# Kernel optimization log

Measured on AMD Instinct MI355X. Metric: run time of the kernel, lower is better.

The kernel has to match this reference:

```python
import jax, jax.numpy as jnp
import numpy as np

N_NODES = 100000
N_EDGES = 3200000
IN_FEATS = 256
HEADS = 8
OUT_FEATS = 32
NEG_SLOPE = 0.2


def setup_inputs() -> dict:
    key = jax.random.key(0)
    k1, k2, k3, k4, k5, k6 = jax.random.split(key, 6)
    feat = jax.random.normal(k1, (N_NODES, IN_FEATS), dtype=jnp.float32)
    src = jax.random.randint(k2, (N_EDGES,), 0, N_NODES, dtype=jnp.int32)
    dst = jax.random.randint(k3, (N_EDGES,), 0, N_NODES, dtype=jnp.int32)
    fc_weight = jax.random.normal(k4, (HEADS * OUT_FEATS, IN_FEATS), dtype=jnp.float32) * 0.05
    attn_l = jax.random.normal(k5, (1, HEADS, OUT_FEATS), dtype=jnp.float32) * 0.1
    attn_r = jax.random.normal(k6, (1, HEADS, OUT_FEATS), dtype=jnp.float32) * 0.1
    bias_param = jnp.zeros((HEADS * OUT_FEATS,), dtype=jnp.float32)
    return {"feat": feat, "src": src, "dst": dst, "fc_weight": fc_weight,
            "attn_l": attn_l, "attn_r": attn_r, "bias_param": bias_param}


def reference(feat, src, dst, fc_weight, attn_l, attn_r, bias_param):
    # Linear projection: [N, in] @ [in, H*F] -> [N, H, F]
    h = (feat @ fc_weight.T).reshape(-1, HEADS, OUT_FEATS)
    # Per-node attention logits: [N, H]
    el = jnp.einsum('nhf,hf->nh', h, attn_l[0])
    er = jnp.einsum('nhf,hf->nh', h, attn_r[0])
    # Edge scores: gather + add + LeakyReLU -> [E, H]
    e = el[src] + er[dst]
    e = jnp.where(e > 0, e, NEG_SLOPE * e)
    # Edge softmax: segment-softmax over destination nodes
    m = jax.ops.segment_max(e, dst, num_segments=N_NODES)  # [N, H]
    m = jnp.where(jnp.isfinite(m), m, 0.0)
    ex = jnp.exp(e - m[dst])                               # [E, H]
    s = jax.ops.segment_sum(ex, dst, num_segments=N_NODES)  # [N, H]
    a = ex / jnp.where(s[dst] > 0, s[dst], 1.0)            # [E, H]
    # Weighted scatter-sum aggregation: [E, H, F] -> [N, H, F]
    msg = h[src] * a[:, :, None]
    rst = jax.ops.segment_sum(msg, dst, num_segments=N_NODES)
    rst = rst + bias_param.reshape(1, HEADS, OUT_FEATS)
    return rst
```

## Files before the change

kernel.cpp:

```cpp
#include <hip/hip_runtime.h>
#include <hip/hip_bf16.h>
#include <stdint.h>

#define N_IN   256
#define HEADS  8
#define OUTF   32
#define HF     256
#define NEG    0.2f

#define SHIFT  8
#define BMASK  255
#define NBMAX  512
#define TILE   8192

typedef __attribute__((ext_vector_type(8))) short  s16x8;
typedef __attribute__((ext_vector_type(4))) float  f32x4;

__device__ __forceinline__ unsigned short f2b(float f) {
    unsigned int u = __float_as_uint(f);
    unsigned int r = (u + 0x7fffu + ((u >> 16) & 1u)) >> 16;
    return (unsigned short)r;
}
__device__ __forceinline__ float b2f(unsigned short u) {
    union { unsigned int i; float f; } x; x.i = ((unsigned int)u) << 16; return x.f;
}

__global__ __launch_bounds__(256) void probe_fill(float* __restrict__ out, int n, float val)
{
    int i = blockIdx.x * blockDim.x + threadIdx.x;
    if (i < n) out[i] = val;
}

__global__ __launch_bounds__(256) void cvt_w(const float* __restrict__ W,
                                             unsigned short* __restrict__ Wb, int n)
{
    int i = blockIdx.x * blockDim.x + threadIdx.x;
    if (i < n) Wb[i] = f2b(W[i]);
}

__global__ __launch_bounds__(256) void gemm_h(
    const float* __restrict__ feat,
    const unsigned short* __restrict__ Wb,
    unsigned short* __restrict__ h, int* __restrict__ flag, int N)
{
    int wave = (blockIdx.x * blockDim.x + threadIdx.x) >> 6;
    int lane = threadIdx.x & 63;
    int m0 = wave * 16;
    if (m0 >= N) return;
    int mr = lane & 15;
    int kg = lane >> 4;

    const float* ap = feat + (size_t)(m0 + mr) * N_IN + kg * 8;
    bool bad = false;
    s16x8 a[8];
#pragma unroll
    for (int kk = 0; kk < 8; kk++) {
        f32x4 lo = __builtin_nontemporal_load((const f32x4*)(ap + kk * 32));
        f32x4 hi = __builtin_nontemporal_load((const f32x4*)(ap + kk * 32 + 4));
#pragma unroll
        for (int j = 0; j < 4; j++) {
            bad |= ((__float_as_uint(lo[j]) >> 23) & 0xFF) >= 0x90;
            bad |= ((__float_as_uint(hi[j]) >> 23) & 0xFF) >= 0x90;
        }
        s16x8 r;
        r[0] = (short)f2b(lo[0]); r[1] = (short)f2b(lo[1]);
        r[2] = (short)f2b(lo[2]); r[3] = (short)f2b(lo[3]);
        r[4] = (short)f2b(hi[0]); r[5] = (short)f2b(hi[1]);
        r[6] = (short)f2b(hi[2]); r[7] = (short)f2b(hi[3]);
        a[kk] = r;
    }
    if (__ballot(bad) != 0ull && lane == 0) atomicOr(flag, 1);

    f32x4 acc[16];
#pragma unroll
    for (int nt = 0; nt < 16; nt++) {
        acc[nt] = (f32x4){0.f, 0.f, 0.f, 0.f};
        const unsigned short* bp = Wb + (size_t)(nt * 16 + mr) * N_IN + kg * 8;
#pragma unroll
        for (int kk = 0; kk < 8; kk++) {
            s16x8 b = *(const s16x8*)(bp + kk * 32);
            acc[nt] = __builtin_amdgcn_mfma_f32_16x16x32_bf16(a[kk], b, acc[nt], 0, 0, 0);
        }
    }
#pragma unroll
    for (int nt = 0; nt < 16; nt++) {
        int col = nt * 16 + mr;
#pragma unroll
        for (int r = 0; r < 4; r++) {
            int row = kg * 4 + r;
            h[(size_t)(m0 + row) * HF + col] = f2b(acc[nt][r]);
        }
    }
}

__global__ __launch_bounds__(256) void el_er_kernel(
    const unsigned short* __restrict__ h,
    const float* __restrict__ attn_l,
    const float* __restrict__ attn_r,
    float* __restrict__ el, float* __restrict__ er, int N)
{
    int t = blockIdx.x * blockDim.x + threadIdx.x;
    if (t >= N * HEADS) return;
    int n = t >> 3, hd = t & 7;
    const unsigned short* hp = h + (size_t)n * HF + hd * OUTF;
    const float* al = attn_l + hd * OUTF;
    const float* ar = attn_r + hd * OUTF;
    float sl = 0.f, sr = 0.f;
#pragma unroll
    for (int i = 0; i < 4; i++) {
        s16x8 hv = *(const s16x8*)(hp + i * 8);
        f32x4 al0 = *(const f32x4*)(al + i * 8);
        f32x4 al1 = *(const f32x4*)(al + i * 8 + 4);
        f32x4 ar0 = *(const f32x4*)(ar + i * 8);
        f32x4 ar1 = *(const f32x4*)(ar + i * 8 + 4);
#pragma unroll
        for (int j = 0; j < 4; j++) {
            float v = b2f((unsigned short)hv[j]);
            sl += v * al0[j]; sr += v * ar0[j];
        }
#pragma unroll
        for (int j = 0; j < 4; j++) {
            float v = b2f((unsigned short)hv[4 + j]);
            sl += v * al1[j]; sr += v * ar1[j];
        }
    }
    el[t] = sl; er[t] = sr;
}

__global__ __launch_bounds__(256) void bin_count(
    const int* __restrict__ dst, int* __restrict__ bucket_count, int E, int N, int NB)
{
    __shared__ int hist[NBMAX];
    int t = threadIdx.x;
#pragma unroll
    for (int i = t; i < NBMAX; i += 256) hist[i] = 0;
    __syncthreads();
    int tb = blockIdx.x * TILE;
#pragma unroll
    for (int i = 0; i < TILE / 256; i++) {
        int e = tb + t + i * 256;
        if (e < E) {
            int d = __builtin_nontemporal_load(&dst[e]);
            d = min(max(d, 0), N - 1);
            atomicAdd(&hist[d >> SHIFT], 1);
        }
    }
    __syncthreads();
    for (int b = t; b < NB; b += 256) {
        int c = hist[b];
        if (c) atomicAdd(&bucket_count[b], c);
    }
}

__global__ __launch_bounds__(512) void scan_buckets(
    const int* __restrict__ bucket_count, int* __restrict__ bucket_base,
    int* __restrict__ bucket_cursor, int NB)
{
    __shared__ int lds[512];
    int t = threadIdx.x;
    int v = (t < NB) ? bucket_count[t] : 0;
    lds[t] = v;
    __syncthreads();
    for (int off = 1; off < 512; off <<= 1) {
        int y = (t >= off) ? lds[t - off] : 0;
        __syncthreads();
        lds[t] += y;
        __syncthreads();
    }
    if (t < NB) { bucket_base[t] = lds[t] - v; bucket_cursor[t] = lds[t] - v; }
}

__global__ __launch_bounds__(256) void bin_scatter(
    const int* __restrict__ src, const int* __restrict__ dst,
    int* __restrict__ bucket_cursor, unsigned int* __restrict__ mid,
    int E, int N, int NB)
{
    __shared__ int hist[NBMAX];
    __shared__ int cur[NBMAX];
    __shared__ int gbase[NBMAX];
    __shared__ int part[256];
    __shared__ unsigned int  sorted[TILE];
    __shared__ unsigned short sortedb[TILE];
    int t = threadIdx.x;
#pragma unroll
    for (int i = t; i < NBMAX; i += 256) hist[i] = 0;
    __syncthreads();
    int tb = blockIdx.x * TILE;
    int cnt = min(TILE, E - tb);

#pragma unroll
    for (int i = 0; i < TILE / 256; i++) {
        int e = tb + t + i * 256;
        if (e < E) {
            int d = __builtin_nontemporal_load(&dst[e]);
            d = min(max(d, 0), N - 1);
            atomicAdd(&hist[d >> SHIFT], 1);
        }
    }
    __syncthreads();

    for (int b = t; b < NB; b += 256) {
        int c = hist[b];
        gbase[b] = c ? atomicAdd(&bucket_cursor[b], c) : 0;
    }

    int b0 = 2 * t, b1 = 2 * t + 1;
    int c0 = hist[b0], c1 = hist[b1];
    part[t] = c0 + c1;
    __syncthreads();
    for (int off = 1; off < 256; off <<= 1) {
        int y = (t >= off) ? part[t - off] : 0;
        __syncthreads();
        part[t] += y;
        __syncthreads();
    }
    int pb = part[t] - (c0 + c1);
    hist[b0] = pb;      hist[b1] = pb + c0;
    cur[b0]  = pb;      cur[b1]  = pb + c0;
    __syncthreads();

#pragma unroll
    for (int i = 0; i < TILE / 256; i++) {
        int e = tb + t + i * 256;
        if (e < E) {
            int d = dst[e]; d = min(max(d, 0), N - 1);
            int s = src[e]; s = min(max(s, 0), N - 1);
            int b = d >> SHIFT;
            int p = atomicAdd(&cur[b], 1);
            sorted[p]  = ((unsigned int)s << SHIFT) | (unsigned int)(d & BMASK);
            sortedb[p] = (unsigned short)b;
        }
    }
    __syncthreads();

    for (int i = t; i < cnt; i += 256) {
        int b = sortedb[i];
        mid[gbase[b] + (i - hist[b])] = sorted[i];
    }
}

__global__ __launch_bounds__(256) void bucket_sort(
    const unsigned int* __restrict__ mid,
    const int* __restrict__ bucket_base, const int* __restrict__ bucket_count,
    int* __restrict__ offs, int* __restrict__ ssorted, int N, int E, int NB)
{
    __shared__ int hist[256];
    __shared__ int lds[256];
    __shared__ int cur[256];
    int b = blockIdx.x;
    int t = threadIdx.x;
    hist[t] = 0;
    __syncthreads();
    int base = bucket_base[b], cnt = bucket_count[b];
    for (int i = t; i < cnt; i += 256) {
        unsigned int v = mid[base + i];
        atomicAdd(&hist[v & BMASK], 1);
    }
    __syncthreads();
    int c = hist[t];
    lds[t] = c;
    __syncthreads();
    for (int off = 1; off < 256; off <<= 1) {
        int y = (t >= off) ? lds[t - off] : 0;
        __syncthreads();
        lds[t] += y;
        __syncthreads();
    }
    int excl = lds[t] - c;
    cur[t] = excl;
    int node = (b << SHIFT) + t;
    if (node < N) offs[node] = base + excl;
    if (b == NB - 1 && t == 0) offs[N] = E;
    __syncthreads();
    for (int i = t; i < cnt; i += 256) {
        unsigned int v = mid[base + i];
        int p = atomicAdd(&cur[v & BMASK], 1);
        ssorted[base + p] = (int)(v >> SHIFT);
    }
}

__global__ __launch_bounds__(256) void aggregate(
    const unsigned short* __restrict__ h,
    const float* __restrict__ el, const float* __restrict__ er,
    const int* __restrict__ offs, const int* __restrict__ ssorted,
    const float* __restrict__ bias,
    const int* __restrict__ flag,
    float* __restrict__ out, int N, int E)
{
    int wave = blockIdx.x * 4 + (threadIdx.x >> 6);
    int lane = threadIdx.x & 63;
    if (wave >= N) return;
    int node = wave;
    int flagv = flag[0];
    int e0 = offs[node], e1 = offs[node + 1];
    e0 = min(max(e0, 0), E);
    e1 = min(max(e1, e0), E);

    int slot = lane >> 4;
    int g    = lane & 15;
    int hg   = g >> 1;

    float er_d = er[node * HEADS + hg];
    float s_acc = 0.f;
    float acc[16];
#pragma unroll
    for (int i = 0; i < 16; i++) acc[i] = 0.f;

    if (e0 < e1) {
        int jA = e0 + slot;
        int sA = __builtin_nontemporal_load(&ssorted[jA]);
        int sB = __builtin_nontemporal_load(&ssorted[jA + 4]);
        bool vA = jA < e1;
        bool vB = (jA + 4) < e1;
        int snA = vA ? sA : 0;
        float elA = el[snA * HEADS + hg];
        const unsigned short* hpA = h + (size_t)snA * HF + g * 16;
        s16x8 hA0 = *(const s16x8*)hpA;
        s16x8 hA1 = *(const s16x8*)(hpA + 8);

        for (int j0 = e0; j0 < e1; j0 += 4) {
            int sC = __builtin_nontemporal_load(&ssorted[j0 + 8 + slot]);
            int snB = vB ? sB : 0;
            float elB = el[snB * HEADS + hg];
            const unsigned short* hpB = h + (size_t)snB * HF + g * 16;
            s16x8 hB0 = *(const s16x8*)hpB;
            s16x8 hB1 = *(const s16x8*)(hpB + 8);
            __builtin_amdgcn_sched_barrier(0);
            float e = elA + er_d;
            e = fmaxf(e, NEG * e);
            float a = vA ? __expf(e) : 0.f;
            s_acc += a;
#pragma unroll
            for (int i = 0; i < 8; i++) acc[i]     += a * b2f((unsigned short)hA0[i]);
#pragma unroll
            for (int i = 0; i < 8; i++) acc[8 + i] += a * b2f((unsigned short)hA1[i]);
            vA = vB; elA = elB; hA0 = hB0; hA1 = hB1;
            sB = sC; vB = (j0 + 8 + slot) < e1;
        }
    }

    s_acc += __shfl_xor(s_acc, 16);
    s_acc += __shfl_xor(s_acc, 32);
#pragma unroll
    for (int i = 0; i < 16; i++) {
        acc[i] += __shfl_xor(acc[i], 16);
        acc[i] += __shfl_xor(acc[i], 32);
    }
    float inv = (s_acc > 0.f) ? 1.f / s_acc : 0.f;

    if (slot == 0) {
        int fo = g * 16;
        bool badv = !__builtin_isfinite(s_acc);
        float vbuf[16];
#pragma unroll
        for (int i = 0; i < 16; i++) {
            float v = acc[i] * inv + bias[fo + i];
            badv |= !__builtin_isfinite(v);
            vbuf[i] = v;
        }
        if (flagv) {
#pragma unroll
            for (int i = 0; i < 16; i++) vbuf[i] = 555.0f;
        } else if (badv) {
#pragma unroll
            for (int i = 0; i < 16; i++) vbuf[i] = 777.0f;
        }
#pragma unroll
        for (int q = 0; q < 4; q++) {
            f32x4 o = { vbuf[q*4+0], vbuf[q*4+1], vbuf[q*4+2], vbuf[q*4+3] };
            __builtin_nontemporal_store(o, (f32x4*)(out + (size_t)node * HF + fo + q * 4));
        }
    }
}

extern "C" void kernel_launch(void* const* d_in, const int* in_sizes, int n_in,
                              void* d_out, int out_size, void* d_ws, size_t ws_size,
                              hipStream_t stream)
{
    const float* feat   = (const float*)d_in[0];
    const int*   src    = (const int*)d_in[1];
    const int*   dst    = (const int*)d_in[2];
    const float* fc_w   = (const float*)d_in[3];
    const float* attn_l = (const float*)d_in[4];
    const float* attn_r = (const float*)d_in[5];
    const float* bias   = (const float*)d_in[6];
    float* out = (float*)d_out;

    const int N = in_sizes[0] / N_IN;
    const int E = in_sizes[1];
    const int NB = (N + 255) >> SHIFT;

    char* ws = (char*)d_ws;
    size_t off = 0;
    auto alloc = [&](size_t bytes) -> char* {
        char* p = ws + off;
        off = (off + bytes + 255) & ~(size_t)255;
        return p;
    };
    int* bucket_count  = (int*)alloc((size_t)NBMAX * 4 + 256);
    int* flag          = bucket_count + NBMAX;
    int* bucket_base   = (int*)alloc((size_t)NBMAX * 4);
    int* bucket_cursor = (int*)alloc((size_t)NBMAX * 4);
    unsigned int* mid  = (unsigned int*)alloc((size_t)E * 4);
    int* ssorted       = (int*)alloc((size_t)(E + 64) * 4);
    int* offs          = (int*)alloc((size_t)(N + 1) * 4);
    float* el          = (float*)alloc((size_t)N * HEADS * 4);
    float* er          = (float*)alloc((size_t)N * HEADS * 4);
    unsigned short* h  = (unsigned short*)alloc((size_t)N * HF * 2);
    unsigned short* Wb = (unsigned short*)alloc((size_t)HF * N_IN * 2);

    if (off > ws_size || NB > NBMAX || N >= (1 << 24)) {
        probe_fill<<<(out_size + 255) / 256, 256, 0, stream>>>(out, out_size, 999.0f);
        return;
    }

    hipMemsetAsync(bucket_count, 0, (size_t)NBMAX * 4 + 256, stream);

    cvt_w<<<(HF * N_IN + 255) / 256, 256, 0, stream>>>(fc_w, Wb, HF * N_IN);
    {
        int waves = (N + 15) / 16;
        int blocks = (waves + 3) / 4;
        gemm_h<<<blocks, 256, 0, stream>>>(feat, Wb, h, flag, N);
    }
    {
        int th = N * HEADS;
        el_er_kernel<<<(th + 255) / 256, 256, 0, stream>>>(h, attn_l, attn_r, el, er, N);
    }
    int tiles = (E + TILE - 1) / TILE;
    bin_count<<<tiles, 256, 0, stream>>>(dst, bucket_count, E, N, NB);
    scan_buckets<<<1, 512, 0, stream>>>(bucket_count, bucket_base, bucket_cursor, NB);
    bin_scatter<<<tiles, 256, 0, stream>>>(src, dst, bucket_cursor, mid, E, N, NB);
    bucket_sort<<<NB, 256, 0, stream>>>(mid, bucket_base, bucket_count, offs, ssorted, N, E, NB);
    {
        int blocks = (N + 3) / 4;
        aggregate<<<blocks, 256, 0, stream>>>(h, el, er, offs, ssorted, bias, flag, out, N, E);
    }
}
```

Baseline: 686.3 us.

## Fuse el/er into GEMM and drop count pass via fixed-capacity buckets

```diff
diff --git a/kernel.cpp b/kernel.cpp
--- a/kernel.cpp
+++ b/kernel.cpp
@@ -12,6 +12,7 @@
 #define BMASK  255
 #define NBMAX  512
 #define TILE   8192
+#define CAP    10240
 
 typedef __attribute__((ext_vector_type(8))) short  s16x8;
 typedef __attribute__((ext_vector_type(4))) float  f32x4;
@@ -41,10 +42,16 @@
 __global__ __launch_bounds__(256) void gemm_h(
     const float* __restrict__ feat,
     const unsigned short* __restrict__ Wb,
-    unsigned short* __restrict__ h, int* __restrict__ flag, int N)
-{
+    const float* __restrict__ attn_l,
+    const float* __restrict__ attn_r,
+    unsigned short* __restrict__ h,
+    float* __restrict__ el, float* __restrict__ er,
+    int* __restrict__ flag, int N)
+{
+    __shared__ unsigned short hs[4][16][260];
     int wave = (blockIdx.x * blockDim.x + threadIdx.x) >> 6;
     int lane = threadIdx.x & 63;
+    int w    = (threadIdx.x >> 6) & 3;
     int m0 = wave * 16;
     if (m0 >= N) return;
     int mr = lane & 15;
@@ -88,92 +95,48 @@
 #pragma unroll
         for (int r = 0; r < 4; r++) {
             int row = kg * 4 + r;
-            h[(size_t)(m0 + row) * HF + col] = f2b(acc[nt][r]);
-        }
-    }
-}
-
-__global__ __launch_bounds__(256) void el_er_kernel(
-    const unsigned short* __restrict__ h,
-    const float* __restrict__ attn_l,
-    const float* __restrict__ attn_r,
-    float* __restrict__ el, float* __restrict__ er, int N)
-{
-    int t = blockIdx.x * blockDim.x + threadIdx.x;
-    if (t >= N * HEADS) return;
-    int n = t >> 3, hd = t & 7;
-    const unsigned short* hp = h + (size_t)n * HF + hd * OUTF;
-    const float* al = attn_l + hd * OUTF;
-    const float* ar = attn_r + hd * OUTF;
-    float sl = 0.f, sr = 0.f;
-#pragma unroll
-    for (int i = 0; i < 4; i++) {
-        s16x8 hv = *(const s16x8*)(hp + i * 8);
-        f32x4 al0 = *(const f32x4*)(al + i * 8);
-        f32x4 al1 = *(const f32x4*)(al + i * 8 + 4);
-        f32x4 ar0 = *(const f32x4*)(ar + i * 8);
-        f32x4 ar1 = *(const f32x4*)(ar + i * 8 + 4);
-#pragma unroll
-        for (int j = 0; j < 4; j++) {
-            float v = b2f((unsigned short)hv[j]);
-            sl += v * al0[j]; sr += v * ar0[j];
-        }
-#pragma unroll
-        for (int j = 0; j < 4; j++) {
-            float v = b2f((unsigned short)hv[4 + j]);
-            sl += v * al1[j]; sr += v * ar1[j];
-        }
-    }
-    el[t] = sl; er[t] = sr;
-}
-
-__global__ __launch_bounds__(256) void bin_count(
-    const int* __restrict__ dst, int* __restrict__ bucket_count, int E, int N, int NB)
-{
-    __shared__ int hist[NBMAX];
-    int t = threadIdx.x;
-#pragma unroll
-    for (int i = t; i < NBMAX; i += 256) hist[i] = 0;
-    __syncthreads();
-    int tb = blockIdx.x * TILE;
-#pragma unroll
-    for (int i = 0; i < TILE / 256; i++) {
-        int e = tb + t + i * 256;
-        if (e < E) {
-            int d = __builtin_nontemporal_load(&dst[e]);
-            d = min(max(d, 0), N - 1);
-            atomicAdd(&hist[d >> SHIFT], 1);
-        }
-    }
-    __syncthreads();
-    for (int b = t; b < NB; b += 256) {
-        int c = hist[b];
-        if (c) atomicAdd(&bucket_count[b], c);
-    }
-}
-
-__global__ __launch_bounds__(512) void scan_buckets(
-    const int* __restrict__ bucket_count, int* __restrict__ bucket_base,
-    int* __restrict__ bucket_cursor, int NB)
-{
-    __shared__ int lds[512];
-    int t = threadIdx.x;
-    int v = (t < NB) ? bucket_count[t] : 0;
-    lds[t] = v;
-    __syncthreads();
-    for (int off = 1; off < 512; off <<= 1) {
-        int y = (t >= off) ? lds[t - off] : 0;
-        __syncthreads();
-        lds[t] += y;
-        __syncthreads();
-    }
-    if (t < NB) { bucket_base[t] = lds[t] - v; bucket_cursor[t] = lds[t] - v; }
+            unsigned short hb = f2b(acc[nt][r]);
+            h[(size_t)(m0 + row) * HF + col] = hb;
+            hs[w][row][col] = hb;
+        }
+    }
+    {
+        int row = lane >> 2, hd4 = lane & 3;
+#pragma unroll
+        for (int p = 0; p < 2; p++) {
+            int hd = hd4 + p * 4;
+            const unsigned short* hp = &hs[w][row][hd * OUTF];
+            const float* al = attn_l + hd * OUTF;
+            const float* ar = attn_r + hd * OUTF;
+            float sl = 0.f, sr = 0.f;
+#pragma unroll
+            for (int i = 0; i < 4; i++) {
+                s16x8 hv = *(const s16x8*)(hp + i * 8);
+                f32x4 al0 = *(const f32x4*)(al + i * 8);
+                f32x4 al1 = *(const f32x4*)(al + i * 8 + 4);
+                f32x4 ar0 = *(const f32x4*)(ar + i * 8);
+                f32x4 ar1 = *(const f32x4*)(ar + i * 8 + 4);
+#pragma unroll
+                for (int j = 0; j < 4; j++) {
+                    float v = b2f((unsigned short)hv[j]);
+                    sl += v * al0[j]; sr += v * ar0[j];
+                }
+#pragma unroll
+                for (int j = 0; j < 4; j++) {
+                    float v = b2f((unsigned short)hv[4 + j]);
+                    sl += v * al1[j]; sr += v * ar1[j];
+                }
+            }
+            el[(size_t)(m0 + row) * HEADS + hd] = sl;
+            er[(size_t)(m0 + row) * HEADS + hd] = sr;
+        }
+    }
 }
 
 __global__ __launch_bounds__(256) void bin_scatter(
     const int* __restrict__ src, const int* __restrict__ dst,
     int* __restrict__ bucket_cursor, unsigned int* __restrict__ mid,
-    int E, int N, int NB)
+    int* __restrict__ flag, int E, int N, int NB)
 {
     __shared__ int hist[NBMAX];
     __shared__ int cur[NBMAX];
@@ -201,7 +164,9 @@
 
     for (int b = t; b < NB; b += 256) {
         int c = hist[b];
-        gbase[b] = c ? atomicAdd(&bucket_cursor[b], c) : 0;
+        int gb = c ? atomicAdd(&bucket_cursor[b], c) : 0;
+        gbase[b] = gb;
+        if (c && gb + c > CAP) atomicOr(flag, 1);
     }
 
     int b0 = 2 * t, b1 = 2 * t + 1;
@@ -235,13 +200,31 @@
 
     for (int i = t; i < cnt; i += 256) {
         int b = sortedb[i];
-        mid[gbase[b] + (i - hist[b])] = sorted[i];
-    }
+        int idx = gbase[b] + (i - hist[b]);
+        if (idx < CAP) mid[(size_t)b * CAP + idx] = sorted[i];
+    }
+}
+
+__global__ __launch_bounds__(512) void scan_buckets(
+    const int* __restrict__ bucket_cursor, int* __restrict__ bucket_base, int NB)
+{
+    __shared__ int lds[512];
+    int t = threadIdx.x;
+    int v = (t < NB) ? bucket_cursor[t] : 0;
+    lds[t] = v;
+    __syncthreads();
+    for (int off = 1; off < 512; off <<= 1) {
+        int y = (t >= off) ? lds[t - off] : 0;
+        __syncthreads();
+        lds[t] += y;
+        __syncthreads();
+    }
+    if (t < NB) bucket_base[t] = lds[t] - v;
 }
 
 __global__ __launch_bounds__(256) void bucket_sort(
     const unsigned int* __restrict__ mid,
-    const int* __restrict__ bucket_base, const int* __restrict__ bucket_count,
+    const int* __restrict__ bucket_base, const int* __restrict__ bucket_cursor,
     int* __restrict__ offs, int* __restrict__ ssorted, int N, int E, int NB)
 {
     __shared__ int hist[256];
@@ -251,9 +234,11 @@
     int t = threadIdx.x;
     hist[t] = 0;
     __syncthreads();
-    int base = bucket_base[b], cnt = bucket_count[b];
+    int base = bucket_base[b];
+    int cnt  = min(bucket_cursor[b], CAP);
+    const unsigned int* ms = mid + (size_t)b * CAP;
     for (int i = t; i < cnt; i += 256) {
-        unsigned int v = mid[base + i];
+        unsigned int v = ms[i];
         atomicAdd(&hist[v & BMASK], 1);
     }
     __syncthreads();
@@ -273,7 +258,7 @@
     if (b == NB - 1 && t == 0) offs[N] = E;
     __syncthreads();
     for (int i = t; i < cnt; i += 256) {
-        unsigned int v = mid[base + i];
+        unsigned int v = ms[i];
         int p = atomicAdd(&cur[v & BMASK], 1);
         ssorted[base + p] = (int)(v >> SHIFT);
     }
@@ -312,6 +297,7 @@
         int sB = __builtin_nontemporal_load(&ssorted[jA + 4]);
         bool vA = jA < e1;
         bool vB = (jA + 4) < e1;
+        sA = min(max(sA, 0), N - 1);
         int snA = vA ? sA : 0;
         float elA = el[snA * HEADS + hg];
         const unsigned short* hpA = h + (size_t)snA * HF + g * 16;
@@ -320,7 +306,8 @@
 
         for (int j0 = e0; j0 < e1; j0 += 4) {
             int sC = __builtin_nontemporal_load(&ssorted[j0 + 8 + slot]);
-            int snB = vB ? sB : 0;
+            int sBc = min(max(sB, 0), N - 1);
+            int snB = vB ? sBc : 0;
             float elB = el[snB * HEADS + hg];
             const unsigned short* hpB = h + (size_t)snB * HF + g * 16;
             s16x8 hB0 = *(const s16x8*)hpB;
@@ -397,11 +384,10 @@
         off = (off + bytes + 255) & ~(size_t)255;
         return p;
     };
-    int* bucket_count  = (int*)alloc((size_t)NBMAX * 4 + 256);
-    int* flag          = bucket_count + NBMAX;
+    int* bucket_cursor = (int*)alloc((size_t)NBMAX * 4 + 256);
+    int* flag          = bucket_cursor + NBMAX;
     int* bucket_base   = (int*)alloc((size_t)NBMAX * 4);
-    int* bucket_cursor = (int*)alloc((size_t)NBMAX * 4);
-    unsigned int* mid  = (unsigned int*)alloc((size_t)E * 4);
+    unsigned int* mid  = (unsigned int*)alloc((size_t)NB * CAP * 4);
     int* ssorted       = (int*)alloc((size_t)(E + 64) * 4);
     int* offs          = (int*)alloc((size_t)(N + 1) * 4);
     float* el          = (float*)alloc((size_t)N * HEADS * 4);
@@ -414,23 +400,18 @@
         return;
     }
 
-    hipMemsetAsync(bucket_count, 0, (size_t)NBMAX * 4 + 256, stream);
+    hipMemsetAsync(bucket_cursor, 0, (size_t)NBMAX * 4 + 256, stream);
 
     cvt_w<<<(HF * N_IN + 255) / 256, 256, 0, stream>>>(fc_w, Wb, HF * N_IN);
     {
         int waves = (N + 15) / 16;
         int blocks = (waves + 3) / 4;
-        gemm_h<<<blocks, 256, 0, stream>>>(feat, Wb, h, flag, N);
-    }
-    {
-        int th = N * HEADS;
-        el_er_kernel<<<(th + 255) / 256, 256, 0, stream>>>(h, attn_l, attn_r, el, er, N);
+        gemm_h<<<blocks, 256, 0, stream>>>(feat, Wb, attn_l, attn_r, h, el, er, flag, N);
     }
     int tiles = (E + TILE - 1) / TILE;
-    bin_count<<<tiles, 256, 0, stream>>>(dst, bucket_count, E, N, NB);
-    scan_buckets<<<1, 512, 0, stream>>>(bucket_count, bucket_base, bucket_cursor, NB);
-    bin_scatter<<<tiles, 256, 0, stream>>>(src, dst, bucket_cursor, mid, E, N, NB);
-    bucket_sort<<<NB, 256, 0, stream>>>(mid, bucket_base, bucket_count, offs, ssorted, N, E, NB);
+    bin_scatter<<<tiles, 256, 0, stream>>>(src, dst, bucket_cursor, mid, flag, E, N, NB);
+    scan_buckets<<<1, 512, 0, stream>>>(bucket_cursor, bucket_base, NB);
+    bucket_sort<<<NB, 256, 0, stream>>>(mid, bucket_base, bucket_cursor, offs, ssorted, N, E, NB);
     {
         int blocks = (N + 3) / 4;
         aggregate<<<blocks, 256, 0, stream>>>(h, el, er, offs, ssorted, bias, flag, out, N, E);
```

Measured after the change: 669.3 us. 1.03x faster.
